# Optimization experiments

Measured on AMD Instinct MI355X. Metric: run time of the kernel, lower is better.

## Reference

```python
import jax, jax.numpy as jnp
import numpy as np
from jax import lax

NPOINT = 512
RADIUS = 0.2
NSAMPLE = 32
BN_EPS = 1e-5


def farthest_point_sample(xyz, npoint):
    # xyz: [B, N, 3] -> centroids: [B, npoint] int32
    # Deterministic init (index 0) instead of torch's randint for reproducibility.
    B, N, _ = xyz.shape
    batch = jnp.arange(B)

    def body(carry, _):
        distance, farthest = carry
        centroid = xyz[batch, farthest][:, None, :]          # [B,1,3]
        dist = jnp.sum((xyz - centroid) ** 2, -1)             # [B,N]
        distance = jnp.minimum(distance, dist)
        new_far = jnp.argmax(distance, axis=-1).astype(jnp.int32)
        return (distance, new_far), farthest

    init = (jnp.full((B, N), 1e10, xyz.dtype), jnp.zeros((B,), jnp.int32))
    _, cents = lax.scan(body, init, None, length=npoint)      # [npoint, B]
    return cents.T


def gather_points(points, idx):
    # points: [B,N,C], idx: [B,...] -> [B,...,C]
    return jax.vmap(lambda p, i: p[i])(points, idx)


def query_ball_point(radius, nsample, xyz, new_xyz):
    # xyz: [B,N,3], new_xyz: [B,S,3] -> idx: [B,S,nsample]
    B, N, _ = xyz.shape
    sqrdists = jnp.sum((new_xyz[:, :, None, :] - xyz[:, None, :, :]) ** 2, -1)  # [B,S,N]
    gidx = jnp.where(sqrdists > radius * radius, N, jnp.arange(N))
    gidx = jnp.sort(gidx, axis=-1)[:, :, :nsample]
    first = gidx[:, :, :1]
    return jnp.where(gidx == N, first, gidx)


def setup_inputs() -> dict:
    key = jax.random.key(0)
    ks = jax.random.split(key, 8)
    B, N, D = 16, 8192, 3
    inp = {
        "xyz": jax.random.uniform(ks[0], (B, N, 3), jnp.float32),
        "points": jax.random.normal(ks[1], (B, N, D), jnp.float32),
    }
    chans = [D + 3, 64, 64, 128]
    for i in range(3):
        cin, cout = chans[i], chans[i + 1]
        inp[f"w{i}"] = jax.random.normal(ks[2 + i], (cout, cin), jnp.float32) / np.sqrt(cin)
        inp[f"b{i}"] = jnp.zeros((cout,), jnp.float32)
        inp[f"g{i}"] = jnp.ones((cout,), jnp.float32)
        inp[f"beta{i}"] = jnp.zeros((cout,), jnp.float32)
    return inp


def _forward(xyz, points, params):
    fps_idx = farthest_point_sample(xyz, NPOINT)               # [B,S]
    new_xyz = gather_points(xyz, fps_idx)                      # [B,S,3]
    idx = query_ball_point(RADIUS, NSAMPLE, xyz, new_xyz)      # [B,S,K]
    grouped_xyz = gather_points(xyz, idx) - new_xyz[:, :, None, :]  # [B,S,K,3]
    grouped_pts = gather_points(points, idx)                   # [B,S,K,D]
    feat = jnp.concatenate([grouped_xyz, grouped_pts], -1)     # [B,S,K,3+D]
    for w, b, g, be in params:
        feat = jnp.einsum('bskc,oc->bsko', feat, w) + b        # 1x1 conv
        mean = jnp.mean(feat, axis=(0, 1, 2))                  # BN (training stats)
        var = jnp.var(feat, axis=(0, 1, 2))
        feat = g * (feat - mean) * lax.rsqrt(var + BN_EPS) + be
        feat = jax.nn.relu(feat)
    new_points = jnp.max(feat, axis=2)                         # max over nsample -> [B,S,Cout]
    return new_xyz, new_points


def reference(xyz, points, w0, b0, g0, beta0, w1, b1, g1, beta1, w2, b2, g2, beta2):
    params = [(w0, b0, g0, beta0), (w1, b1, g1, beta1), (w2, b2, g2, beta2)]
    return _forward(xyz, points, params)
```

## Files before the change

### kernel.cpp

```cpp
#include <hip/hip_runtime.h>
#include <hip/hip_bf16.h>
#include <cstdint>
#include <cstddef>

#define NB 16
#define NN 8192
#define NS 512
#define NK 32
#define NG (NB*NS)
#define GPB 4
#define NBLK (NG/GPB)
#define NPOSI 262144

__device__ __forceinline__ double sq3d(double dx, double dy, double dz){
#pragma clang fp contract(off)
  const double a = dx*dx;
  const double b = dy*dy;
  const double c = dz*dz;
  return (a + b) + c;
}

template<int CTRL>
__device__ __forceinline__ unsigned dpp_umax_step(unsigned v){
  const unsigned o = (unsigned)__builtin_amdgcn_update_dpp(0, (int)v, CTRL, 0xf, 0xf, false);
  return v > o ? v : o;
}
__device__ __forceinline__ unsigned wave_umax63(unsigned v){
  v = dpp_umax_step<0xB1>(v);
  v = dpp_umax_step<0x4E>(v);
  v = dpp_umax_step<0x141>(v);
  v = dpp_umax_step<0x140>(v);
  v = dpp_umax_step<0x142>(v);
  v = dpp_umax_step<0x143>(v);
  return v;
}

__device__ __forceinline__ unsigned mort4(unsigned v){
  return (v & 1u) | ((v & 2u) << 2) | ((v & 4u) << 4) | ((v & 8u) << 6);
}

__global__ __launch_bounds__(1024) void k_morton(const float* __restrict__ xyz,
                                                 int* __restrict__ ord){
  const int b = blockIdx.x;
  const int t = threadIdx.x;
  const float* __restrict__ X = xyz + (size_t)b*NN*3;
  __shared__ unsigned sHist[4096];
  __shared__ unsigned sWT[16];
  for (int k=t; k<4096; k+=1024) sHist[k] = 0u;
  __syncthreads();
  unsigned code[8];
#pragma unroll
  for (int j=0;j<8;++j){
    const int p = t + 1024*j;
    const float x=X[p*3+0], y=X[p*3+1], z=X[p*3+2];
    const unsigned ix=(unsigned)min(15,max(0,(int)(x*16.f)));
    const unsigned iy=(unsigned)min(15,max(0,(int)(y*16.f)));
    const unsigned iz=(unsigned)min(15,max(0,(int)(z*16.f)));
    code[j] = mort4(ix) | (mort4(iy)<<1) | (mort4(iz)<<2);
    atomicAdd(&sHist[code[j]], 1u);
  }
  __syncthreads();
  {
    const uint4 h = ((const uint4*)sHist)[t];
    const unsigned l1=h.x, l2=h.x+h.y, l3=h.x+h.y+h.z, tot=l3+h.w;
    unsigned inc = tot;
    const int lane = t & 63;
#pragma unroll
    for (int d2=1; d2<64; d2<<=1){
      const unsigned v = __shfl_up(inc, d2);
      if (lane >= d2) inc += v;
    }
    const unsigned wexc = inc - tot;
    if (lane == 63) sWT[t>>6] = inc;
    __syncthreads();
    if (t == 0){
      unsigned run = 0;
#pragma unroll
      for (int k=0;k<16;++k){ const unsigned v=sWT[k]; sWT[k]=run; run+=v; }
    }
    __syncthreads();
    const unsigned base = sWT[t>>6] + wexc;
    uint4 o; o.x=base; o.y=base+l1; o.z=base+l2; o.w=base+l3;
    ((uint4*)sHist)[t] = o;
  }
  __syncthreads();
#pragma unroll
  for (int j=0;j<8;++j){
    const unsigned pos = atomicAdd(&sHist[code[j]], 1u);
    ord[(size_t)b*NN + pos] = t + 1024*j;
  }
}

__global__ __launch_bounds__(1024) void k_fps(const float* __restrict__ xyz,
                                              const int* __restrict__ ord,
                                              float* __restrict__ newxyz){
  const int b = blockIdx.x;
  const int t = threadIdx.x;
  const float* __restrict__ X = xyz + (size_t)b*NN*3;

  __shared__ float4 sP[NN];
  __shared__ unsigned sM32[2];
  __shared__ unsigned long long sMax64[2];
  __shared__ int sIdx[2];
  __shared__ int sSel[NS];

  int oidx[8];
#pragma unroll
  for (int j=0;j<8;++j){
    const int p = t + 1024*j;
    sP[p] = make_float4(X[p*3+0], X[p*3+1], X[p*3+2], 0.f);
    oidx[j] = ord[(size_t)b*NN + 8*t + j];
  }
  if (t < 2){ sM32[t]=0u; sMax64[t]=0ull; sIdx[t]=0x7fffffff; }
  __syncthreads();

  float px[8], py[8], pz[8], thr[8];
  double dd[8];
#pragma unroll
  for (int j=0;j<8;++j){
    const float4 q = sP[oidx[j]];
    px[j]=q.x; py[j]=q.y; pz[j]=q.z;
    dd[j]=1e10;
    thr[j]=fmaf(1e10f, 0x1p-19f, 1e10f);
  }
  float ctx=0.f, cty=0.f, ctz=0.f;
#pragma unroll
  for (int j=0;j<8;++j){ ctx+=px[j]; cty+=py[j]; ctz+=pz[j]; }
  ctx*=0.125f; cty*=0.125f; ctz*=0.125f;
  float r2m = 0.f;
#pragma unroll
  for (int j=0;j<8;++j){
    const float ax=px[j]-ctx, ay=py[j]-cty, az=pz[j]-ctz;
    r2m = fmaxf(r2m, fmaf(az,az,fmaf(ay,ay,ax*ax)));
  }
  const float rT = sqrtf(r2m)*(1.0f+0x1p-18f) + 0x1p-20f;

  double tmax = 1e10;
  float  tmax32 = 1e10f;
  int tio = oidx[0], ts = 0;
#pragma unroll
  for (int j=1;j<8;++j) if (oidx[j] < tio){ tio = oidx[j]; ts = j; }
  float skipgate = tmax32*(1.0f+0x1p-14f);

  int f = 0;
  const int lane = t & 63;

  for (int i=0;i<NS;++i){
    if (t == 0) sSel[i] = f;
    if (i == NS-1) break;
    const int par = i & 1;

    const float4 cf = sP[f];
    const float cx=cf.x, cy=cf.y, cz=cf.z;

    const float bx=cx-ctx, by=cy-cty, bz=cz-ctz;
    const float ddc = fmaf(bz,bz,fmaf(by,by,bx*bx));
    const float dcc = sqrtf(ddc);
    float s = dcc - rT; s = s - dcc*0x1p-16f;
    const bool engage = !(s > 0.f && s*s >= skipgate);

    if (engage){
      float e[8]; float mmin = 1e30f;
#pragma unroll
      for (int j=0;j<8;++j){
        const float ax=px[j]-cx, ay=py[j]-cy, az=pz[j]-cz;
        const float d32 = fmaf(az, az, fmaf(ay, ay, ax*ax));
        e[j] = d32 - thr[j];
        mmin = fminf(mmin, e[j]);
      }
      if (__builtin_expect(mmin <= 0.f, 0)){
        const double cxd=(double)cx, cyd=(double)cy, czd=(double)cz;
        bool needscan = false;
#pragma unroll
        for (int j=0;j<8;++j){
          if (e[j] <= 0.f){
            const double d64 = sq3d((double)px[j]-cxd, (double)py[j]-cyd, (double)pz[j]-czd);
            const double nd = fmin(dd[j], d64);
            needscan |= (j == ts) | (nd == tmax);
            dd[j] = nd;
            const float nd32 = (float)nd;
            thr[j] = fmaf(nd32, 0x1p-19f, nd32);
          }
        }
        if (needscan){
          double tm = dd[0]; int io = oidx[0]; int s0 = 0;
#pragma unroll
          for (int j=1;j<8;++j)
            if (dd[j] > tm || (dd[j] == tm && oidx[j] < io)){ tm=dd[j]; io=oidx[j]; s0=j; }
          tmax=tm; tio=io; ts=s0; tmax32=(float)tm;
          skipgate = tmax32*(1.0f+0x1p-14f);
        }
      }
    }

    const unsigned myb = __float_as_uint(tmax32);
    const unsigned vb = wave_umax63(myb);
    if (lane == 63) atomicMax(&sM32[par], vb);
    __syncthreads();

    const bool cand = (myb == sM32[par]);
    if (cand) atomicMax(&sMax64[par], (unsigned long long)__double_as_longlong(tmax));
    __syncthreads();

    if (cand && (unsigned long long)__double_as_longlong(tmax) == sMax64[par])
      atomicMin(&sIdx[par], tio);
    if (t == 0){ sM32[par^1]=0u; sMax64[par^1]=0ull; sIdx[par^1]=0x7fffffff; }
    __syncthreads();
    f = sIdx[par];
  }
  __syncthreads();
  if (t < NS){
    const int id = sSel[t];
    const float4 cf = sP[id];
    float* o = newxyz + ((size_t)b*NS + t)*3;
    o[0]=cf.x; o[1]=cf.y; o[2]=cf.z;
  }
}

__global__ __launch_bounds__(256) void k_ball(const float* __restrict__ xyz,
                                              const float* __restrict__ newxyz,
                                              int* __restrict__ idx){
  const int w = (blockIdx.x << 2) + (threadIdx.x >> 6);
  const int lane = threadIdx.x & 63;
  const int b = w >> 9;
  const float* __restrict__ C = newxyz + (size_t)w*3;
  const float cxf=C[0], cyf=C[1], czf=C[2];
  const double cx=(double)cxf, cy=(double)cyf, cz=(double)czf;
  const float* __restrict__ X = xyz + (size_t)b*NN*3;
  int* __restrict__ out = idx + (size_t)w*NK;
  const double R2 = 0.2*0.2;
  const float r2lo = 0.04f*(1.0f - 0x1p-16f);
  const float r2hi = 0.04f*(1.0f + 0x1p-16f);
  int count = 0, first = 0;
  for (int base=0; base<NN && count<NK; base+=64){
    const int p = base + lane;
    const float ax=X[p*3+0]-cxf, ay=X[p*3+1]-cyf, az=X[p*3+2]-czf;
    const float d32 = fmaf(az, az, fmaf(ay, ay, ax*ax));
    bool q;
    if (d32 <= r2lo)      q = true;
    else if (d32 > r2hi)  q = false;
    else {
      const double d = sq3d((double)X[p*3+0]-cx, (double)X[p*3+1]-cy, (double)X[p*3+2]-cz);
      q = !(d > R2);
    }
    const unsigned long long m = __ballot(q);
    if (q){
      const int pos = count + __popcll(m & ((1ull<<lane)-1ull));
      if (pos < NK) out[pos] = p;
    }
    if (count == 0 && m) first = base + __builtin_ctzll(m);
    count += __popcll(m);
  }
  if (lane >= count && lane < NK) out[lane] = first;
}

__device__ __forceinline__ void stats_reduce(
    float v[4][8], float* __restrict__ sRed, int t, int tp, int tc, int blk,
    int chtot, int choff, bool domm,
    float* __restrict__ pS, float* __restrict__ pQ,
    float* __restrict__ mxp, float* __restrict__ mnp)
{
  __syncthreads();
  float S=0.f, Q=0.f;
  for (int m=0;m<4;++m){
#pragma unroll
    for (int i=0;i<8;++i) sRed[tp*68 + tc*8 + i] = v[m][i];
    __syncthreads();
    if (t < 64){
      float mxv = -3.402823466e38f, mnv = 3.402823466e38f;
#pragma unroll
      for (int j=0;j<32;++j){
        const float x = sRed[j*68 + t];
        S += x; Q += x*x;
        mxv = fmaxf(mxv,x); mnv = fminf(mnv,x);
      }
      if (domm){
        const int gg = blk*GPB + m;
        mxp[(size_t)gg*128 + choff + t] = mxv;
        mnp[(size_t)gg*128 + choff + t] = mnv;
      }
    }
    __syncthreads();
  }
  if (t < 64){
    pS[(size_t)blk*chtot + choff + t] = S;
    pQ[(size_t)blk*chtot + choff + t] = Q;
  }
}

__device__ __forceinline__ void mm64(const float* __restrict__ sXl,
                                     const float* __restrict__ sWl,
                                     int tp, int tc, float v[4][8]){
#pragma unroll 4
  for (int k=0;k<64;++k){
    float xv[4], wv[8];
#pragma unroll
    for (int m=0;m<4;++m) xv[m] = sXl[(tp+32*m)*65 + k];
#pragma unroll
    for (int i=0;i<8;++i) wv[i] = sWl[(tc*8+i)*65 + k];
#pragma unroll
    for (int m=0;m<4;++m)
#pragma unroll
      for (int i=0;i<8;++i) v[m][i] += xv[m]*wv[i];
  }
}

template<int DEPTH>
__global__ __launch_bounds__(256) void k_pass(
    const float* __restrict__ xyz, const float* __restrict__ points,
    const float* __restrict__ newxyz, const int* __restrict__ idx,
    const float* __restrict__ w0, const float* __restrict__ b0,
    const float* __restrict__ w1, const float* __restrict__ b1,
    const float* __restrict__ w2, const float* __restrict__ b2,
    const float* __restrict__ ac,
    float* __restrict__ pS, float* __restrict__ pQ,
    float* __restrict__ mxp, float* __restrict__ mnp)
{
  __shared__ float smem[(DEPTH>=1) ? 14784 : 2304];
  float* sX0 = smem;
  float* sW0 = smem + 1024;
  float* sV  = smem + 1600;
  float* sRed= smem;
  float* sB2 = smem + 2176;
  float* sW1 = smem + 2304;
  float* sX  = smem + 6464;

  const int t = threadIdx.x;
  const int blk = blockIdx.x;
  const int tc = t & 7, tp = t >> 3;

  for (int i=t;i<384;i+=256) sW0[(i/6)*9 + (i%6)] = w0[i];
  if (t < 64) sV[t] = b0[t];
  if constexpr (DEPTH >= 1){
    if (t < 64){ sV[64+t]=ac[t]; sV[128+t]=ac[64+t]; sV[192+t]=b1[t]; }
    for (int i=t;i<4096;i+=256) sW1[(i>>6)*65 + (i&63)] = w1[i];
  }
  if constexpr (DEPTH == 2){
    if (t < 64){ sV[256+t]=ac[128+t]; sV[320+t]=ac[192+t]; }
    if (t < 128) sB2[t] = b2[t];
  }

  {
    const int pos = t & 127;
    const int gg = blk*GPB + (pos >> 5);
    const int b  = gg >> 9;
    const int id = idx[gg*NK + (pos & 31)];
    if (t < 128){
      const float* __restrict__ P = xyz + ((size_t)b*NN + id)*3;
      const float* __restrict__ C = newxyz + (size_t)gg*3;
      sX0[pos*8+0] = P[0]-C[0];
      sX0[pos*8+1] = P[1]-C[1];
      sX0[pos*8+2] = P[2]-C[2];
    } else {
      const float* __restrict__ P = points + ((size_t)b*NN + id)*3;
      sX0[pos*8+3] = P[0];
      sX0[pos*8+4] = P[1];
      sX0[pos*8+5] = P[2];
    }
  }
  __syncthreads();

  float v[4][8];
#pragma unroll
  for (int m=0;m<4;++m){
    const int pos = tp + 32*m;
    float xr[6];
#pragma unroll
    for (int c=0;c<6;++c) xr[c] = sX0[pos*8+c];
#pragma unroll
    for (int i=0;i<8;++i){
      const int ch = tc*8+i;
      float acc = sV[ch];
#pragma unroll
      for (int c=0;c<6;++c) acc += sW0[ch*9+c]*xr[c];
      v[m][i] = acc;
    }
  }

  if constexpr (DEPTH == 0){
    stats_reduce(v, sRed, t, tp, tc, blk, 64, 0, false, pS, pQ, mxp, mnp);
    return;
  } else {
#pragma unroll
    for (int m=0;m<4;++m){
      const int pos = tp + 32*m;
#pragma unroll
      for (int i=0;i<8;++i){
        const int ch = tc*8+i;
        sX[pos*65+ch] = fmaxf(sV[64+ch]*v[m][i] + sV[128+ch], 0.f);
      }
    }
    __syncthreads();
#pragma unroll
    for (int m=0;m<4;++m)
#pragma unroll
      for (int i=0;i<8;++i) v[m][i] = sV[192 + tc*8 + i];
    mm64(sX, sW1, tp, tc, v);

    if constexpr (DEPTH == 1){
      stats_reduce(v, sRed, t, tp, tc, blk, 64, 0, false, pS, pQ, mxp, mnp);
      return;
    } else {
      __syncthreads();
#pragma unroll
      for (int m=0;m<4;++m){
        const int pos = tp + 32*m;
#pragma unroll
        for (int i=0;i<8;++i){
          const int ch = tc*8+i;
          sX[pos*65+ch] = fmaxf(sV[256+ch]*v[m][i] + sV[320+ch], 0.f);
        }
      }
      __syncthreads();
      for (int o=0;o<2;++o){
        for (int i=t;i<4096;i+=256) sW1[(i>>6)*65 + (i&63)] = w2[o*4096 + i];
        __syncthreads();
#pragma unroll
        for (int m=0;m<4;++m)
#pragma unroll
          for (int i=0;i<8;++i) v[m][i] = sB2[o*64 + tc*8 + i];
        mm64(sX, sW1, tp, tc, v);
        stats_reduce(v, sRed, t, tp, tc, blk, 128, o*64, true, pS, pQ, mxp, mnp);
      }
      return;
    }
  }
}

__global__ __launch_bounds__(1024) void k_stats(const float* __restrict__ pS, const float* __restrict__ pQ,
                                                const float* __restrict__ g, const float* __restrict__ beta,
                                                float* __restrict__ a, float* __restrict__ c, int CH){
  __shared__ float sS[1024], sQ[1024];
  const int t = threadIdx.x;
  const int ch = t & (CH-1);
  const int seg = t / CH;
  const int SEG = 1024 / CH;
  const int rows = NBLK / SEG;
  float S=0.f, Q=0.f;
  const int j0 = seg*rows;
#pragma unroll 4
  for (int r=0;r<rows;++r){
    const size_t o = (size_t)(j0+r)*CH + ch;
    S += pS[o]; Q += pQ[o];
  }
  sS[t]=S; sQ[t]=Q;
  __syncthreads();
  if (t < CH){
    float aS=0.f, aQ=0.f;
    for (int s2=0;s2<SEG;++s2){ aS += sS[s2*CH+ch]; aQ += sQ[s2*CH+ch]; }
    const float mean = aS * (1.f/(float)NPOSI);
    const float var  = fmaxf(aQ * (1.f/(float)NPOSI) - mean*mean, 0.f);
    const float av = g[ch] * rsqrtf(var + 1e-5f);
    a[ch] = av;
    c[ch] = beta[ch] - mean*av;
  }
}

__global__ __launch_bounds__(256) void k_final(const float* __restrict__ mxp, const float* __restrict__ mnp,
                                               const float* __restrict__ a, const float* __restrict__ c,
                                               float* __restrict__ out){
  const int i = blockIdx.x*256 + threadIdx.x;
  const int ch = i & 127;
  const float av = a[ch], cv = c[ch];
  const float vv = (av >= 0.f) ? mxp[i] : mnp[i];
  out[i] = fmaxf(av*vv + cv, 0.f);
}

extern "C" void kernel_launch(void* const* d_in, const int* in_sizes, int n_in,
                              void* d_out, int out_size, void* d_ws, size_t ws_size,
                              hipStream_t stream){
  (void)in_sizes; (void)n_in; (void)out_size;
  const float* xyz    = (const float*)d_in[0];
  const float* points = (const float*)d_in[1];
  const float* w0 = (const float*)d_in[2];
  const float* b0 = (const float*)d_in[3];
  const float* g0 = (const float*)d_in[4];
  const float* be0= (const float*)d_in[5];
  const float* w1 = (const float*)d_in[6];
  const float* b1 = (const float*)d_in[7];
  const float* g1 = (const float*)d_in[8];
  const float* be1= (const float*)d_in[9];
  const float* w2 = (const float*)d_in[10];
  const float* b2 = (const float*)d_in[11];
  const float* g2 = (const float*)d_in[12];
  const float* be2= (const float*)d_in[13];

  float* out_newxyz = (float*)d_out;
  float* out_newpts = out_newxyz + (size_t)NB*NS*3;

  char* ws = (char*)d_ws;
  int*   idx = (int*)ws;
  float* ac  = (float*)(ws + (1u<<20));
  float* pS  = (float*)(ws + (1u<<20) + 4096);
  float* pQ  = pS + (size_t)NBLK*128;
  float* mxp = pQ + (size_t)NBLK*128;
  float* mnp = mxp + (size_t)NG*128;
  const size_t need = (1u<<20) + 4096 + (size_t)2*NBLK*128*4 + (size_t)2*NG*128*4;
  if (ws_size < need) return;

  int* ord = idx;

  k_morton<<<NB, 1024, 0, stream>>>(xyz, ord);
  k_fps  <<<NB, 1024, 0, stream>>>(xyz, ord, out_newxyz);
  k_ball <<<NG/4, 256, 0, stream>>>(xyz, out_newxyz, idx);

  k_pass<0><<<NBLK,256,0,stream>>>(xyz,points,out_newxyz,idx,w0,b0,w1,b1,w2,b2,ac,pS,pQ,mxp,mnp);
  k_stats<<<1,1024,0,stream>>>(pS,pQ,g0,be0, ac+0,   ac+64,  64);
  k_pass<1><<<NBLK,256,0,stream>>>(xyz,points,out_newxyz,idx,w0,b0,w1,b1,w2,b2,ac,pS,pQ,mxp,mnp);
  k_stats<<<1,1024,0,stream>>>(pS,pQ,g1,be1, ac+128, ac+192, 64);
  k_pass<2><<<NBLK,256,0,stream>>>(xyz,points,out_newxyz,idx,w0,b0,w1,b1,w2,b2,ac,pS,pQ,mxp,mnp);
  k_stats<<<1,1024,0,stream>>>(pS,pQ,g2,be2, ac+256, ac+384, 128);
  k_final<<<(NG*128)/256,256,0,stream>>>(mxp,mnp,ac+256,ac+384,out_newpts);
}
```

Baseline: 1.186 ms.

## Replace FPS barrier-based argmax with flag-based wave-leader reduction

```diff
diff --git a/kernel.cpp b/kernel.cpp
--- a/kernel.cpp
+++ b/kernel.cpp
@@ -34,6 +34,13 @@
   v = dpp_umax_step<0x143>(v);
   return v;
 }
+__device__ __forceinline__ unsigned grp16_umax(unsigned v){
+  v = dpp_umax_step<0xB1>(v);
+  v = dpp_umax_step<0x4E>(v);
+  v = dpp_umax_step<0x141>(v);
+  v = dpp_umax_step<0x140>(v);
+  return v;
+}
 
 __device__ __forceinline__ unsigned mort4(unsigned v){
   return (v & 1u) | ((v & 2u) << 2) | ((v & 4u) << 4) | ((v & 8u) << 6);
@@ -99,9 +106,11 @@
   const float* __restrict__ X = xyz + (size_t)b*NN*3;
 
   __shared__ float4 sP[NN];
-  __shared__ unsigned sM32[2];
-  __shared__ unsigned long long sMax64[2];
-  __shared__ int sIdx[2];
+  __shared__ unsigned long long sWv64[16];
+  __shared__ int      sWi[16];
+  __shared__ unsigned sWf[16];
+  __shared__ unsigned sTag[16];
+  __shared__ unsigned sF;
   __shared__ int sSel[NS];
 
   int oidx[8];
@@ -111,7 +120,8 @@
     sP[p] = make_float4(X[p*3+0], X[p*3+1], X[p*3+2], 0.f);
     oidx[j] = ord[(size_t)b*NN + 8*t + j];
   }
-  if (t < 2){ sM32[t]=0u; sMax64[t]=0ull; sIdx[t]=0x7fffffff; }
+  if (t < 16) sTag[t] = 0u;
+  if (t == 0) sF = 0u;
   __syncthreads();
 
   float px[8], py[8], pz[8], thr[8];
@@ -143,12 +153,11 @@
   float skipgate = tmax32*(1.0f+0x1p-14f);
 
   int f = 0;
-  const int lane = t & 63;
+  const int lane = t & 63, wid = t >> 6;
 
   for (int i=0;i<NS;++i){
     if (t == 0) sSel[i] = f;
     if (i == NS-1) break;
-    const int par = i & 1;
 
     const float4 cf = sP[f];
     const float cx=cf.x, cy=cf.y, cz=cf.z;
@@ -194,19 +203,65 @@
     }
 
     const unsigned myb = __float_as_uint(tmax32);
-    const unsigned vb = wave_umax63(myb);
-    if (lane == 63) atomicMax(&sM32[par], vb);
-    __syncthreads();
-
-    const bool cand = (myb == sM32[par]);
-    if (cand) atomicMax(&sMax64[par], (unsigned long long)__double_as_longlong(tmax));
-    __syncthreads();
-
-    if (cand && (unsigned long long)__double_as_longlong(tmax) == sMax64[par])
-      atomicMin(&sIdx[par], tio);
-    if (t == 0){ sM32[par^1]=0u; sMax64[par^1]=0ull; sIdx[par^1]=0x7fffffff; }
-    __syncthreads();
-    f = sIdx[par];
+    const unsigned wm = (unsigned)__builtin_amdgcn_readlane((int)wave_umax63(myb), 63);
+    const unsigned long long mask = __ballot(myb == wm);
+    int writer;
+    if (__builtin_expect(__popcll(mask) == 1, 1)){
+      writer = (int)__builtin_ctzll(mask);
+    } else {
+      double bestv = -1.0; int bestid = 0x7fffffff;
+      unsigned long long mm = mask;
+      while (mm){
+        const int l = (int)__builtin_ctzll(mm);
+        const double v = __shfl(tmax, l);
+        const int   id = __shfl(tio, l);
+        if (v > bestv || (v == bestv && id < bestid)){ bestv=v; bestid=id; }
+        mm &= mm - 1;
+      }
+      writer = (int)__builtin_ctzll(__ballot(tmax == bestv && tio == bestid));
+    }
+    if (lane == writer){
+      sWv64[wid] = (unsigned long long)__double_as_longlong(tmax);
+      sWi[wid]   = tio;
+      sWf[wid]   = wm;
+      __hip_atomic_store(&sTag[wid], (unsigned)(i+1),
+                         __ATOMIC_RELEASE, __HIP_MEMORY_SCOPE_WORKGROUP);
+    }
+
+    if (wid == 0){
+      const int w = lane & 15;
+      while (__hip_atomic_load(&sTag[w], __ATOMIC_ACQUIRE,
+                               __HIP_MEMORY_SCOPE_WORKGROUP) != (unsigned)(i+1)) {}
+      const double vb = __longlong_as_double((long long)sWv64[w]);
+      const int    io = sWi[w];
+      const unsigned wf = sWf[w];
+      const unsigned m32 = grp16_umax(wf);
+      const unsigned long long cm = __ballot(wf == m32) & 0xFFFFull;
+      int fnew;
+      if (__builtin_expect(__popcll(cm) == 1, 1)){
+        fnew = __shfl(io, (int)__builtin_ctzll(cm));
+      } else {
+        double bestv = -1.0; int bestid = 0x7fffffff;
+        unsigned long long mm = cm;
+        while (mm){
+          const int l = (int)__builtin_ctzll(mm);
+          const double v = __shfl(vb, l);
+          const int   id = __shfl(io, l);
+          if (v > bestv || (v == bestv && id < bestid)){ bestv=v; bestid=id; }
+          mm &= mm - 1;
+        }
+        fnew = bestid;
+      }
+      if (lane == 0)
+        __hip_atomic_store(&sF, (((unsigned)(i+1))<<13) | (unsigned)fnew,
+                           __ATOMIC_RELEASE, __HIP_MEMORY_SCOPE_WORKGROUP);
+    }
+
+    unsigned v;
+    do {
+      v = __hip_atomic_load(&sF, __ATOMIC_ACQUIRE, __HIP_MEMORY_SCOPE_WORKGROUP);
+    } while ((v >> 13) != (unsigned)(i+1));
+    f = (int)(v & 8191u);
   }
   __syncthreads();
   if (t < NS){
```

After: 1.162 ms. -2.0%, faster.
